# Optimization experiments

Measured on AMD Instinct MI355X. Metric: run time of the kernel, lower is better.

## Reference

```python
import jax, jax.numpy as jnp
import numpy as np

B = 4096          # batch size (scaled up from source's 16)
INPUT_AXIS = 784
LATENT_DIM = 2


def _pdist(x):
    # pairwise euclidean distances in itertools.combinations order (row-major upper triangle)
    sq = jnp.sum(x * x, axis=1)                      # [B]
    d2 = sq[:, None] + sq[None, :] - 2.0 * (x @ x.T)  # [B,B]
    i, j = jnp.triu_indices(x.shape[0], k=1)
    return jnp.sqrt(jnp.maximum(d2[i, j], 0.0))       # [B*(B-1)/2]


def setup_inputs() -> dict:
    key = jax.random.key(0)
    ks = jax.random.split(key, 17)
    dims = [(400, 784), (200, 400), (50, 200), (2, 50),
            (50, 2), (200, 50), (400, 200), (784, 400)]
    names = ['fc1', 'fc1_1', 'fc1_2', 'fc2', 'fc3', 'fc3_1', 'fc3_2', 'fc4']
    inp = {'x': jax.random.uniform(ks[0], (B, 1, 28, 28), dtype=jnp.float32)}
    for idx, (nm, (o, i)) in enumerate(zip(names, dims)):
        bound = 1.0 / np.sqrt(i)
        inp[nm + '_w'] = jax.random.uniform(ks[1 + 2 * idx], (o, i), jnp.float32, -bound, bound)
        inp[nm + '_b'] = jax.random.uniform(ks[2 + 2 * idx], (o,), jnp.float32, -bound, bound)
    return inp


def reference(x, fc1_w, fc1_b, fc1_1_w, fc1_1_b, fc1_2_w, fc1_2_b, fc2_w, fc2_b,
              fc3_w, fc3_b, fc3_1_w, fc3_1_b, fc3_2_w, fc3_2_b, fc4_w, fc4_b):
    lin = lambda h, w, b: h @ w.T + b
    lrelu = jax.nn.leaky_relu  # default slope 0.01, matches F.leaky_relu
    x2 = x.reshape(-1, INPUT_AXIS)                       # [B,784]
    h = lrelu(lin(x2, fc1_w, fc1_b))
    h = lrelu(lin(h, fc1_1_w, fc1_1_b))
    h = lrelu(lin(h, fc1_2_w, fc1_2_b))                  # encoder out [B,50]
    z = lin(jnp.tanh(h), fc2_w, fc2_b)                   # [B,2]
    y = lrelu(lin(z, fc3_w, fc3_b))
    y = lrelu(lin(y, fc3_1_w, fc3_1_b))
    y = lrelu(lin(y, fc3_2_w, fc3_2_b))
    y = jax.nn.sigmoid(lin(y, fc4_w, fc4_b))             # [B,784]
    y_img = y.reshape(B, 1, 28, 28)
    in_diff = _pdist(x2)
    lat_diff = _pdist(z)
    out_diff = _pdist(y.reshape(B, INPUT_AXIS))
    return (y_img, in_diff, lat_diff, out_diff, z)
```

## Files before the change

### kernel.cpp

```cpp
#include <hip/hip_runtime.h>
#include <math.h>

#define NB 4096
#define DIMX 784

typedef __attribute__((ext_vector_type(8))) short bf16x8;
typedef __attribute__((ext_vector_type(4))) float f32x4;

__device__ __forceinline__ float lrelu_f(float v) { return v >= 0.f ? v : 0.01f * v; }

__device__ __forceinline__ void split1(float x, short& hi_s, short& lo_s) {
    unsigned u = __float_as_uint(x);
    unsigned hib = (u + 0x7FFFu + ((u >> 16) & 1u)) & 0xFFFF0000u;
    float hif = __uint_as_float(hib);
    float lo = x - hif;
    unsigned ul = __float_as_uint(lo);
    unsigned lob = (ul + 0x7FFFu + ((ul >> 16) & 1u)) >> 16;
    hi_s = (short)(hib >> 16);
    lo_s = (short)lob;
}

#define GLL(srcp, dstp) __builtin_amdgcn_global_load_lds( \
    (const __attribute__((address_space(1))) void*)(srcp), \
    (__attribute__((address_space(3))) void*)(dstp), 16, 0, 0)


__global__ __launch_bounds__(256) void prep_all(
    const float* __restrict__ w1, const float* __restrict__ w11,
    const float* __restrict__ w32, const float* __restrict__ w4,
    short* __restrict__ o1, short* __restrict__ o11,
    short* __restrict__ o32, short* __restrict__ o4,
    const float* __restrict__ X, short* __restrict__ Xs,
    float* __restrict__ sqx, float* __restrict__ sqy)
{
    const int bid = blockIdx.x;
    const int t = threadIdx.x;
    if (bid < 3920) {
        const float* W; short* O; int N, K, NP, KP, base;
        if (bid < 1600)      { W = w1;  O = o1;  N = 400; K = 784; NP = 512; KP = 800; base = 0; }
        else if (bid < 2016) { W = w11; O = o11; N = 200; K = 400; NP = 256; KP = 416; base = 1600; }
        else if (bid < 2464) { W = w32; O = o32; N = 400; K = 200; NP = 512; KP = 224; base = 2016; }
        else                 { W = w4;  O = o4;  N = 784; K = 400; NP = 896; KP = 416; base = 2464; }
        const int idx = (bid - base) * 256 + t;
        if (idx >= NP * KP) return;
        const int r = idx / KP, k = idx - r * KP;
        short hi = 0, lo = 0;
        if (r < N && k < K) split1(W[(size_t)r * K + k], hi, lo);
        O[(size_t)r * 2 * KP + k]      = hi;
        O[(size_t)r * 2 * KP + KP + k] = lo;
    } else {
        const int r = bid - 3920;
        float s = 0.f;
        if (t < 200) {
            const int k0 = t * 4;
            short h[4] = {0, 0, 0, 0}, l[4] = {0, 0, 0, 0};
            if (k0 < 784) {
                float4 v = *(const float4*)(X + (size_t)r * 784 + k0);
                split1(v.x, h[0], l[0]); split1(v.y, h[1], l[1]);
                split1(v.z, h[2], l[2]); split1(v.w, h[3], l[3]);
                s = v.x * v.x + v.y * v.y + v.z * v.z + v.w * v.w;
            }
            *(uint2*)&Xs[(size_t)r * 1600 + k0]       = *(const uint2*)h;
            *(uint2*)&Xs[(size_t)r * 1600 + 800 + k0] = *(const uint2*)l;
        }
        __shared__ float red[256];
        red[t] = s;
        __syncthreads();
        for (int off = 128; off > 0; off >>= 1) {
            if (t < off) red[t] += red[t + off];
            __syncthreads();
        }
        if (t == 0) { sqx[r] = red[0]; sqy[r] = 0.f; }
    }
}

template<int ACT, bool WF32, bool WSPLIT, bool WROWSQ>
__global__ __launch_bounds__(256) void gemm3_64(
    const short* __restrict__ As_g, const short* __restrict__ Ws_g,
    const float* __restrict__ bias, float* __restrict__ C,
    short* __restrict__ Cs, int N, int KPi, int nchunk, int KPo,
    float* __restrict__ sqy)
{
    __shared__ short L[2][12288];
    const int tid = threadIdx.x;
    const int w = tid >> 6, lane = tid & 63;
    const int wc = w;
    const int m0 = blockIdx.y * 64, n0 = blockIdx.x * 128;
    const int frow = lane & 15;
    const int fk_sw = (((lane >> 4) ^ ((lane >> 1) & 3))) * 8;
    const int srow = tid >> 2;
    const int scol_sw = (((tid & 3) ^ ((tid >> 3) & 3))) * 8;
    const int RS = 2 * KPi;
    const int ld0 = w * 512;

    const short* gA  = As_g + (size_t)(m0 + srow) * RS + scol_sw;
    const short* gB0 = Ws_g + (size_t)(n0 + srow) * RS + scol_sw;
    const short* gB1 = gB0 + (size_t)64 * RS;

    f32x4 acc[4][2] = {};

    auto stage = [&](int buf, int km) {
        GLL(gA  + km,       &L[buf][ld0]);
        GLL(gA  + KPi + km, &L[buf][2048 + ld0]);
        GLL(gB0 + km,       &L[buf][4096 + ld0]);
        GLL(gB1 + km,       &L[buf][6144 + ld0]);
        GLL(gB0 + KPi + km, &L[buf][8192 + ld0]);
        GLL(gB1 + KPi + km, &L[buf][10240 + ld0]);
    };

    stage(0, 0);
    asm volatile("s_waitcnt vmcnt(0)" ::: "memory");
    __builtin_amdgcn_s_barrier();
    int buf = 0;
    #pragma unroll 1
    for (int cc = 0; cc < nchunk; ++cc) {
        if (cc + 1 < nchunk) {
            stage(buf ^ 1, (cc + 1) * 32);
            asm volatile("s_waitcnt vmcnt(6)" ::: "memory");
        } else {
            asm volatile("s_waitcnt vmcnt(0)" ::: "memory");
        }
        __builtin_amdgcn_s_barrier();

        bf16x8 ah[4], al[4], bh[2], bl[2];
        #pragma unroll
        for (int m = 0; m < 4; ++m) {
            const int ro = (m * 16 + frow) * 32 + fk_sw;
            ah[m] = *(const bf16x8*)&L[buf][ro];
            al[m] = *(const bf16x8*)&L[buf][2048 + ro];
        }
        #pragma unroll
        for (int n = 0; n < 2; ++n) {
            const int ro = (wc * 32 + n * 16 + frow) * 32 + fk_sw;
            bh[n] = *(const bf16x8*)&L[buf][4096 + ro];
            bl[n] = *(const bf16x8*)&L[buf][8192 + ro];
        }
        #pragma unroll
        for (int m = 0; m < 4; ++m)
            #pragma unroll
            for (int n = 0; n < 2; ++n) {
                acc[m][n] = __builtin_amdgcn_mfma_f32_16x16x32_bf16(ah[m], bh[n], acc[m][n], 0, 0, 0);
                acc[m][n] = __builtin_amdgcn_mfma_f32_16x16x32_bf16(ah[m], bl[n], acc[m][n], 0, 0, 0);
                acc[m][n] = __builtin_amdgcn_mfma_f32_16x16x32_bf16(al[m], bh[n], acc[m][n], 0, 0, 0);
            }
        __builtin_amdgcn_s_barrier();
        buf ^= 1;
    }

    const int col0 = lane & 15;
    const int row4 = (lane >> 4) * 4;

    float* rowsum = (float*)&L[0][0];
    if (WROWSQ) {
        __syncthreads();
        if (tid < 64) rowsum[tid] = 0.f;
        __syncthreads();
    }

    #pragma unroll
    for (int m = 0; m < 4; ++m) {
        #pragma unroll
        for (int r = 0; r < 4; ++r) {
            const int gm = m0 + m * 16 + row4 + r;
            float vsq = 0.f;
            #pragma unroll
            for (int n = 0; n < 2; ++n) {
                const int gn = n0 + wc * 32 + n * 16 + col0;
                float v = 0.f;
                if (gn < N) {
                    v = acc[m][n][r] + bias[gn];
                    if (ACT == 1)      v = lrelu_f(v);
                    else if (ACT == 2) v = 1.f / (1.f + expf(-v));
                }
                if (WF32 && gn < N) C[(size_t)gm * N + gn] = v;
                if (WSPLIT && gn < KPo) {
                    short hi, lo; split1(v, hi, lo);
                    Cs[(size_t)gm * 2 * KPo + gn]       = hi;
                    Cs[(size_t)gm * 2 * KPo + KPo + gn] = lo;
                }
                if (WROWSQ) vsq = fmaf(v, v, vsq);
            }
            if (WROWSQ) atomicAdd(&rowsum[m * 16 + row4 + r], vsq);
        }
    }
    if (WROWSQ) {
        __syncthreads();
        if (tid < 64) atomicAdd(&sqy[m0 + tid], rowsum[tid]);
    }
}

__global__ __launch_bounds__(256) void fused_mid(
    const float* __restrict__ h2, const float* __restrict__ W12,
    const float* __restrict__ b12, const float* __restrict__ W2,
    const float* __restrict__ b2,  const float* __restrict__ W3,
    const float* __restrict__ b3,  const float* __restrict__ W31,
    const float* __restrict__ b31, float* __restrict__ z_out,
    short* __restrict__ y2s)
{
    __shared__ float wbuf[200 * 51];
    __shared__ float hl[16 * 201];
    __shared__ float h3l[16 * 51];
    __shared__ float y1l[16 * 51];
    __shared__ float zl[16 * 2];
    __shared__ float w2l[100], w3l[100];
    __shared__ float b12l[50], b2l[2], b3l[50], b31l[200];
    const int t = threadIdx.x;
    const int r0 = blockIdx.x * 16;

    for (int i = t; i < 50 * 200; i += 256) { int n = i / 200, k = i - n * 200; wbuf[n * 201 + k] = W12[i]; }
    for (int i = t; i < 16 * 200; i += 256) { int r = i / 200, k = i - r * 200; hl[r * 201 + k] = h2[(size_t)(r0 + r) * 200 + k]; }
    for (int i = t; i < 100; i += 256) { w2l[i] = W2[i]; w3l[i] = W3[i]; }
    if (t < 50)  { b12l[t] = b12[t]; b3l[t] = b3[t]; }
    if (t < 2)   b2l[t] = b2[t];
    if (t < 200) b31l[t] = b31[t];
    __syncthreads();

    for (int i = t; i < 16 * 50; i += 256) {
        int r = i / 50, n = i - r * 50;
        float s = b12l[n];
        #pragma unroll 4
        for (int k = 0; k < 200; ++k) s = fmaf(hl[r * 201 + k], wbuf[n * 201 + k], s);
        h3l[r * 51 + n] = tanhf(lrelu_f(s));
    }
    __syncthreads();

    if (t < 32) {
        int r = t >> 1, n = t & 1;
        float s = b2l[n];
        #pragma unroll
        for (int k = 0; k < 50; ++k) s = fmaf(h3l[r * 51 + k], w2l[n * 50 + k], s);
        zl[r * 2 + n] = s;
        z_out[(size_t)(r0 + r) * 2 + n] = s;
    }
    for (int i = t; i < 200 * 50; i += 256) { int n = i / 50, k = i - n * 50; wbuf[n * 51 + k] = W31[i]; }
    __syncthreads();

    for (int i = t; i < 16 * 50; i += 256) {
        int r = i / 50, n = i - r * 50;
        float s = fmaf(zl[r * 2], w3l[n * 2], fmaf(zl[r * 2 + 1], w3l[n * 2 + 1], b3l[n]));
        y1l[r * 51 + n] = lrelu_f(s);
    }
    __syncthreads();

    for (int i = t; i < 16 * 224; i += 256) {
        int r = i / 224, n = i - r * 224;
        float v = 0.f;
        if (n < 200) {
            float s = b31l[n];
            #pragma unroll
            for (int k = 0; k < 50; ++k) s = fmaf(y1l[r * 51 + k], wbuf[n * 51 + k], s);
            v = lrelu_f(s);
        }
        short hi, lo; split1(v, hi, lo);
        const size_t gm = r0 + r;
        y2s[gm * 448 + n]       = hi;
        y2s[gm * 448 + 224 + n] = lo;
    }
}

__global__ __launch_bounds__(256, 4) void pdist_all(
    const short* __restrict__ xs, const short* __restrict__ ys,
    const float* __restrict__ sqx, const float* __restrict__ sqy,
    const float* __restrict__ Z, float* __restrict__ in_diff,
    float* __restrict__ out_diff, float* __restrict__ lat_diff)
{
    __shared__ short L[4][4096];
    const int tid = threadIdx.x;
    const int orig = blockIdx.x;

    if (orig < 528) {
        const int b = (orig & 7) * 66 + (orig >> 3);
        int rem = b, ti = 0;
        while (rem >= 32 - ti) { rem -= 32 - ti; ++ti; }
        const int tj = ti + rem;

        const int w = tid >> 6, lane = tid & 63;
        const int wr = w >> 1, wc = w & 1;
        const int frow = lane & 15;
        const int fk_sw = (((lane >> 4) ^ ((lane >> 1) & 3))) * 8;
        const int srow = tid >> 2;
        const int scol_sw = (((tid & 3) ^ ((tid >> 3) & 3))) * 8;
        const int i0 = ti * 128, j0 = tj * 128;
        const int ld0 = w * 512;

        const short* gA = ys + (size_t)(i0 + srow) * 1600 + scol_sw;
        const short* gB = ys + (size_t)(j0 + srow) * 1600 + scol_sw;
        const size_t half = (size_t)64 * 1600;

        f32x4 acc[4][4] = {};

        #pragma unroll 1
        for (int cc = 0; cc < 25; ++cc) {
            const int km = cc * 32;
            __syncthreads();
            GLL(gA + km,       &L[0][ld0]);   GLL(gA + half + km,       &L[0][2048 + ld0]);
            GLL(gB + km,       &L[2][ld0]);   GLL(gB + half + km,       &L[2][2048 + ld0]);
            GLL(gA + 800 + km, &L[1][ld0]);   GLL(gA + half + 800 + km, &L[1][2048 + ld0]);
            GLL(gB + 800 + km, &L[3][ld0]);   GLL(gB + half + 800 + km, &L[3][2048 + ld0]);
            __syncthreads();

            bf16x8 ah[4], bh[4];
            #pragma unroll
            for (int m = 0; m < 4; ++m)
                ah[m] = *(const bf16x8*)&L[0][(wr * 64 + m * 16 + frow) * 32 + fk_sw];
            #pragma unroll
            for (int n = 0; n < 4; ++n)
                bh[n] = *(const bf16x8*)&L[2][(wc * 64 + n * 16 + frow) * 32 + fk_sw];
            #pragma unroll
            for (int m = 0; m < 4; ++m)
                #pragma unroll
                for (int n = 0; n < 4; ++n)
                    acc[m][n] = __builtin_amdgcn_mfma_f32_16x16x32_bf16(ah[m], bh[n], acc[m][n], 0, 0, 0);

            bf16x8 al[4], bl[4];
            #pragma unroll
            for (int n = 0; n < 4; ++n)
                bl[n] = *(const bf16x8*)&L[3][(wc * 64 + n * 16 + frow) * 32 + fk_sw];
            #pragma unroll
            for (int m = 0; m < 4; ++m)
                #pragma unroll
                for (int n = 0; n < 4; ++n)
                    acc[m][n] = __builtin_amdgcn_mfma_f32_16x16x32_bf16(ah[m], bl[n], acc[m][n], 0, 0, 0);
            #pragma unroll
            for (int m = 0; m < 4; ++m)
                al[m] = *(const bf16x8*)&L[1][(wr * 64 + m * 16 + frow) * 32 + fk_sw];
            #pragma unroll
            for (int m = 0; m < 4; ++m)
                #pragma unroll
                for (int n = 0; n < 4; ++n)
                    acc[m][n] = __builtin_amdgcn_mfma_f32_16x16x32_bf16(al[m], bh[n], acc[m][n], 0, 0, 0);
        }

        const int col0 = lane & 15;
        const int row4 = (lane >> 4) * 4;
        float sqj_v[4];
        #pragma unroll
        for (int n = 0; n < 4; ++n)
            sqj_v[n] = sqy[j0 + wc * 64 + n * 16 + col0];

        #pragma unroll
        for (int m = 0; m < 4; ++m) {
            #pragma unroll
            for (int r = 0; r < 4; ++r) {
                const int gi = i0 + wr * 64 + m * 16 + row4 + r;
                const float sqi = sqy[gi];
                const int rowbase = (gi * (2 * NB - 1 - gi)) / 2 - gi - 1;
                #pragma unroll
                for (int n = 0; n < 4; ++n) {
                    const int gj = j0 + wc * 64 + n * 16 + col0;
                    if (gj > gi) {
                        float d2 = sqi + sqj_v[n] - 2.f * acc[m][n][r];
                        out_diff[rowbase + gj] = sqrtf(fmaxf(d2, 0.f));
                    }
                }
            }
        }
    } else if (orig < 1056) {
        const int o = orig - 528;
        const int b = (o & 7) * 66 + (o >> 3);
        int rem = b, ti = 0;
        while (rem >= 32 - ti) { rem -= 32 - ti; ++ti; }
        const int tj = ti + rem;

        const int w = tid >> 6, lane = tid & 63;
        const int wr = w >> 1, wc = w & 1;
        const int frow = lane & 15;
        const int fk_sw = (((lane >> 4) ^ ((lane >> 1) & 3))) * 8;
        const int srow = tid >> 2;
        const int scol_sw = (((tid & 3) ^ ((tid >> 3) & 3))) * 8;
        const int i0 = ti * 128, j0 = tj * 128;
        const int ld0 = w * 512;

        const short* gA = xs + (size_t)(i0 + srow) * 1600 + scol_sw;
        const short* gB = xs + (size_t)(j0 + srow) * 1600 + scol_sw;
        const size_t half = (size_t)64 * 1600;

        f32x4 acc[4][4] = {};

        auto stage = [&](int buf, int km) {
            short* dA = buf ? &L[2][0] : &L[0][0];
            short* dB = buf ? &L[3][0] : &L[1][0];
            GLL(gA + km,        dA + ld0);   GLL(gA + half + km, dA + 2048 + ld0);
            GLL(gB + km,        dB + ld0);   GLL(gB + half + km, dB + 2048 + ld0);
        };

        stage(0, 0);
        asm volatile("s_waitcnt vmcnt(0)" ::: "memory");
        __builtin_amdgcn_s_barrier();
        int buf = 0;
        #pragma unroll 1
        for (int cc = 0; cc < 25; ++cc) {
            if (cc < 24) {
                stage(buf ^ 1, (cc + 1) * 32);
                asm volatile("s_waitcnt vmcnt(4)" ::: "memory");
            } else {
                asm volatile("s_waitcnt vmcnt(0)" ::: "memory");
            }
            __builtin_amdgcn_s_barrier();

            const short* SA = buf ? &L[2][0] : &L[0][0];
            const short* SB = buf ? &L[3][0] : &L[1][0];
            bf16x8 a[4], bb[4];
            #pragma unroll
            for (int m = 0; m < 4; ++m)
                a[m] = *(const bf16x8*)&SA[(wr * 64 + m * 16 + frow) * 32 + fk_sw];
            #pragma unroll
            for (int n = 0; n < 4; ++n)
                bb[n] = *(const bf16x8*)&SB[(wc * 64 + n * 16 + frow) * 32 + fk_sw];
            #pragma unroll
            for (int m = 0; m < 4; ++m)
                #pragma unroll
                for (int n = 0; n < 4; ++n)
                    acc[m][n] = __builtin_amdgcn_mfma_f32_16x16x32_bf16(a[m], bb[n], acc[m][n], 0, 0, 0);
            __builtin_amdgcn_s_barrier();
            buf ^= 1;
        }

        const int col0 = lane & 15;
        const int row4 = (lane >> 4) * 4;
        float sqj_v[4];
        #pragma unroll
        for (int n = 0; n < 4; ++n)
            sqj_v[n] = sqx[j0 + wc * 64 + n * 16 + col0];
        #pragma unroll
        for (int m = 0; m < 4; ++m) {
            #pragma unroll
            for (int r = 0; r < 4; ++r) {
                const int gi = i0 + wr * 64 + m * 16 + row4 + r;
                const float sqi = sqx[gi];
                const int rowbase = (gi * (2 * NB - 1 - gi)) / 2 - gi - 1;
                #pragma unroll
                for (int n = 0; n < 4; ++n) {
                    const int gj = j0 + wc * 64 + n * 16 + col0;
                    if (gj > gi) {
                        float d2 = sqi + sqj_v[n] - 2.f * acc[m][n][r];
                        in_diff[rowbase + gj] = sqrtf(fmaxf(d2, 0.f));
                    }
                }
            }
        }
    } else {
        const int o = orig - 1056;
        const int b = (o & 7) * 66 + (o >> 3);
        int rem = b, ti = 0;
        while (rem >= 32 - ti) { rem -= 32 - ti; ++ti; }
        const int tj = ti + rem;
        const int i0 = ti * 128, j0 = tj * 128;

        float* zi = (float*)&L[0][0];
        float* zj = (float*)&L[0][512];
        if (tid < 128) {
            *(float2*)&zi[tid * 2] = *(const float2*)&Z[(size_t)(i0 + tid) * 2];
        } else {
            const int r = tid - 128;
            *(float2*)&zj[r * 2] = *(const float2*)&Z[(size_t)(j0 + r) * 2];
        }
        __syncthreads();

        const int ty = tid >> 4;
        const int tx = tid & 15;
        #pragma unroll
        for (int ii = 0; ii < 8; ++ii) {
            const int li = ty * 8 + ii;
            const int gi = i0 + li;
            const int rowbase = (gi * (2 * NB - 1 - gi)) / 2 - gi - 1;
            const float zi0 = zi[li * 2], zi1 = zi[li * 2 + 1];
            #pragma unroll
            for (int jj = 0; jj < 8; ++jj) {
                const int lj = tx * 8 + jj;
                const int gj = j0 + lj;
                if (gj > gi) {
                    float d0 = zi0 - zj[lj * 2];
                    float d1 = zi1 - zj[lj * 2 + 1];
                    lat_diff[rowbase + gj] = sqrtf(fmaf(d0, d0, d1 * d1));
                }
            }
        }
    }
}

extern "C" void kernel_launch(void* const* d_in, const int* in_sizes, int n_in,
                              void* d_out, int out_size, void* d_ws, size_t ws_size,
                              hipStream_t stream)
{
    const float* x       = (const float*)d_in[0];
    const float* fc1_w   = (const float*)d_in[1];
    const float* fc1_b   = (const float*)d_in[2];
    const float* fc11_w  = (const float*)d_in[3];
    const float* fc11_b  = (const float*)d_in[4];
    const float* fc12_w  = (const float*)d_in[5];
    const float* fc12_b  = (const float*)d_in[6];
    const float* fc2_w   = (const float*)d_in[7];
    const float* fc2_b   = (const float*)d_in[8];
    const float* fc3_w   = (const float*)d_in[9];
    const float* fc3_b   = (const float*)d_in[10];
    const float* fc31_w  = (const float*)d_in[11];
    const float* fc31_b  = (const float*)d_in[12];
    const float* fc32_w  = (const float*)d_in[13];
    const float* fc32_b  = (const float*)d_in[14];
    const float* fc4_w   = (const float*)d_in[15];
    const float* fc4_b   = (const float*)d_in[16];

    float* out = (float*)d_out;
    float* y        = out;
    float* in_diff  = out + 3211264;
    float* lat_diff = out + 11597824;
    float* out_diff = out + 19984384;
    float* z        = out + 28370944;

    float* ws   = (float*)d_ws;
    float* h2   = ws;
    float* h3u  = h2  + (size_t)4096 * 200;
    float* y1u  = h3u + (size_t)4096 * 50;
    float* sqx  = y1u + (size_t)4096 * 50;
    float* sqy  = sqx + 4096;
    short* xs   = (short*)(sqy + 4096);
    short* ys   = xs  + (size_t)NB * 1600;
    short* w1s  = ys  + (size_t)NB * 1600;
    short* w11s = w1s  + (size_t)512 * 1600;
    short* w32s = w11s + (size_t)256 * 832;
    short* w4s  = w32s + (size_t)512 * 448;
    short* h1s  = w4s  + (size_t)896 * 832;
    short* y3s  = h1s;
    short* y2s  = h1s  + (size_t)4096 * 832;

    const dim3 blk(256);

    prep_all<<<dim3(8016), blk, 0, stream>>>(
        fc1_w, fc11_w, fc32_w, fc4_w, w1s, w11s, w32s, w4s, x, xs, sqx, sqy);
    gemm3_64<1, false, true, false><<<dim3(4, 64), blk, 0, stream>>>(
        xs, w1s, fc1_b, nullptr, h1s, 400, 800, 25, 416, nullptr);
    gemm3_64<1, true, false, false><<<dim3(2, 64), blk, 0, stream>>>(
        h1s, w11s, fc11_b, h2, nullptr, 200, 416, 13, 0, nullptr);
    fused_mid<<<dim3(256), blk, 0, stream>>>(
        h2, fc12_w, fc12_b, fc2_w, fc2_b, fc3_w, fc3_b, fc31_w, fc31_b, z, y2s);
    gemm3_64<1, false, true, false><<<dim3(4, 64), blk, 0, stream>>>(
        y2s, w32s, fc32_b, nullptr, y3s, 400, 224, 7, 416, nullptr);
    gemm3_64<2, true, true, true><<<dim3(7, 64), blk, 0, stream>>>(
        y3s, w4s, fc4_b, y, ys, 784, 416, 13, 800, sqy);
    pdist_all<<<dim3(1584), blk, 0, stream>>>(
        xs, ys, sqx, sqy, z, in_diff, out_diff, lat_diff);
}
```

Before: 225.9 us.

## Co-schedule input pdist tiles with the fc1 GEMM in one launch

Computing in_diff depends only on x, so its 528 tile blocks now run in the same launch as the fc1 GEMM (new fc1_mix kernel, 784 blocks). The final pdist kernel keeps only the output and latent distance work. The aim is to fill the GPU during the small fc1 GEMM (256 blocks) and shorten the long tail of the last kernel. fc1 uses a dedicated 64x128 split-bf16 tile with three MFMAs per step. The mixed kernel's larger LDS footprint (48KB) may lower occupancy for the pdist blocks.

```diff
diff --git a/kernel.cpp b/kernel.cpp
--- a/kernel.cpp
+++ b/kernel.cpp
@@ -189,6 +189,181 @@
     }
 }
 
+__global__ __launch_bounds__(256) void fc1_mix(
+    const short* __restrict__ xs, const short* __restrict__ w1s,
+    const float* __restrict__ fc1_b, short* __restrict__ h1s,
+    const float* __restrict__ sqx, float* __restrict__ in_diff)
+{
+    __shared__ short L[24576];
+    const int tid = threadIdx.x;
+    const int w = tid >> 6, lane = tid & 63;
+    const int frow = lane & 15;
+    const int fk_sw = (((lane >> 4) ^ ((lane >> 1) & 3))) * 8;
+    const int srow = tid >> 2;
+    const int scol_sw = (((tid & 3) ^ ((tid >> 3) & 3))) * 8;
+    const int ld0 = w * 512;
+    const int col0 = lane & 15;
+    const int row4 = (lane >> 4) * 4;
+    const int bid = blockIdx.x;
+
+    if (bid < 256) {
+        const int wc = w;
+        const int m0 = (bid >> 2) * 64, n0 = (bid & 3) * 128;
+        const int RS = 1600;
+
+        const short* gA  = xs  + (size_t)(m0 + srow) * RS + scol_sw;
+        const short* gB0 = w1s + (size_t)(n0 + srow) * RS + scol_sw;
+        const short* gB1 = gB0 + (size_t)64 * RS;
+
+        f32x4 acc[4][2] = {};
+
+        auto stage = [&](int buf, int km) {
+            short* B = L + buf * 12288;
+            GLL(gA  + km,       B + ld0);
+            GLL(gA  + 800 + km, B + 2048 + ld0);
+            GLL(gB0 + km,       B + 4096 + ld0);
+            GLL(gB1 + km,       B + 6144 + ld0);
+            GLL(gB0 + 800 + km, B + 8192 + ld0);
+            GLL(gB1 + 800 + km, B + 10240 + ld0);
+        };
+
+        stage(0, 0);
+        asm volatile("s_waitcnt vmcnt(0)" ::: "memory");
+        __builtin_amdgcn_s_barrier();
+        int buf = 0;
+        #pragma unroll 1
+        for (int cc = 0; cc < 25; ++cc) {
+            if (cc < 24) {
+                stage(buf ^ 1, (cc + 1) * 32);
+                asm volatile("s_waitcnt vmcnt(6)" ::: "memory");
+            } else {
+                asm volatile("s_waitcnt vmcnt(0)" ::: "memory");
+            }
+            __builtin_amdgcn_s_barrier();
+
+            const short* B = L + buf * 12288;
+            bf16x8 ah[4], al[4], bh[2], bl[2];
+            #pragma unroll
+            for (int m = 0; m < 4; ++m) {
+                const int ro = (m * 16 + frow) * 32 + fk_sw;
+                ah[m] = *(const bf16x8*)&B[ro];
+                al[m] = *(const bf16x8*)&B[2048 + ro];
+            }
+            #pragma unroll
+            for (int n = 0; n < 2; ++n) {
+                const int ro = (wc * 32 + n * 16 + frow) * 32 + fk_sw;
+                bh[n] = *(const bf16x8*)&B[4096 + ro];
+                bl[n] = *(const bf16x8*)&B[8192 + ro];
+            }
+            #pragma unroll
+            for (int m = 0; m < 4; ++m)
+                #pragma unroll
+                for (int n = 0; n < 2; ++n) {
+                    acc[m][n] = __builtin_amdgcn_mfma_f32_16x16x32_bf16(ah[m], bh[n], acc[m][n], 0, 0, 0);
+                    acc[m][n] = __builtin_amdgcn_mfma_f32_16x16x32_bf16(ah[m], bl[n], acc[m][n], 0, 0, 0);
+                    acc[m][n] = __builtin_amdgcn_mfma_f32_16x16x32_bf16(al[m], bh[n], acc[m][n], 0, 0, 0);
+                }
+            __builtin_amdgcn_s_barrier();
+            buf ^= 1;
+        }
+
+        #pragma unroll
+        for (int m = 0; m < 4; ++m) {
+            #pragma unroll
+            for (int r = 0; r < 4; ++r) {
+                const int gm = m0 + m * 16 + row4 + r;
+                #pragma unroll
+                for (int n = 0; n < 2; ++n) {
+                    const int gn = n0 + wc * 32 + n * 16 + col0;
+                    float v = 0.f;
+                    if (gn < 400) v = lrelu_f(acc[m][n][r] + fc1_b[gn]);
+                    if (gn < 416) {
+                        short hi, lo; split1(v, hi, lo);
+                        h1s[(size_t)gm * 832 + gn]       = hi;
+                        h1s[(size_t)gm * 832 + 416 + gn] = lo;
+                    }
+                }
+            }
+        }
+    } else {
+        const int o = bid - 256;
+        const int b = (o & 7) * 66 + (o >> 3);
+        int rem = b, ti = 0;
+        while (rem >= 32 - ti) { rem -= 32 - ti; ++ti; }
+        const int tj = ti + rem;
+
+        const int wr = w >> 1, wc = w & 1;
+        const int i0 = ti * 128, j0 = tj * 128;
+
+        const short* gA = xs + (size_t)(i0 + srow) * 1600 + scol_sw;
+        const short* gB = xs + (size_t)(j0 + srow) * 1600 + scol_sw;
+        const size_t half = (size_t)64 * 1600;
+
+        f32x4 acc[4][4] = {};
+
+        auto stage = [&](int buf, int km) {
+            short* dA = buf ? L + 8192  : L + 0;
+            short* dB = buf ? L + 12288 : L + 4096;
+            GLL(gA + km,        dA + ld0);   GLL(gA + half + km, dA + 2048 + ld0);
+            GLL(gB + km,        dB + ld0);   GLL(gB + half + km, dB + 2048 + ld0);
+        };
+
+        stage(0, 0);
+        asm volatile("s_waitcnt vmcnt(0)" ::: "memory");
+        __builtin_amdgcn_s_barrier();
+        int buf = 0;
+        #pragma unroll 1
+        for (int cc = 0; cc < 25; ++cc) {
+            if (cc < 24) {
+                stage(buf ^ 1, (cc + 1) * 32);
+                asm volatile("s_waitcnt vmcnt(4)" ::: "memory");
+            } else {
+                asm volatile("s_waitcnt vmcnt(0)" ::: "memory");
+            }
+            __builtin_amdgcn_s_barrier();
+
+            const short* SA = buf ? L + 8192  : L + 0;
+            const short* SB = buf ? L + 12288 : L + 4096;
+            bf16x8 a[4], bb[4];
+            #pragma unroll
+            for (int m = 0; m < 4; ++m)
+                a[m] = *(const bf16x8*)&SA[(wr * 64 + m * 16 + frow) * 32 + fk_sw];
+            #pragma unroll
+            for (int n = 0; n < 4; ++n)
+                bb[n] = *(const bf16x8*)&SB[(wc * 64 + n * 16 + frow) * 32 + fk_sw];
+            #pragma unroll
+            for (int m = 0; m < 4; ++m)
+                #pragma unroll
+                for (int n = 0; n < 4; ++n)
+                    acc[m][n] = __builtin_amdgcn_mfma_f32_16x16x32_bf16(a[m], bb[n], acc[m][n], 0, 0, 0);
+            __builtin_amdgcn_s_barrier();
+            buf ^= 1;
+        }
+
+        float sqj_v[4];
+        #pragma unroll
+        for (int n = 0; n < 4; ++n)
+            sqj_v[n] = sqx[j0 + wc * 64 + n * 16 + col0];
+        #pragma unroll
+        for (int m = 0; m < 4; ++m) {
+            #pragma unroll
+            for (int r = 0; r < 4; ++r) {
+                const int gi = i0 + wr * 64 + m * 16 + row4 + r;
+                const float sqi = sqx[gi];
+                const int rowbase = (gi * (2 * NB - 1 - gi)) / 2 - gi - 1;
+                #pragma unroll
+                for (int n = 0; n < 4; ++n) {
+                    const int gj = j0 + wc * 64 + n * 16 + col0;
+                    if (gj > gi) {
+                        float d2 = sqi + sqj_v[n] - 2.f * acc[m][n][r];
+                        in_diff[rowbase + gj] = sqrtf(fmaxf(d2, 0.f));
+                    }
+                }
+            }
+        }
+    }
+}
+
 __global__ __launch_bounds__(256) void fused_mid(
     const float* __restrict__ h2, const float* __restrict__ W12,
     const float* __restrict__ b12, const float* __restrict__ W2,
@@ -258,11 +433,10 @@
     }
 }
 
-__global__ __launch_bounds__(256, 4) void pdist_all(
-    const short* __restrict__ xs, const short* __restrict__ ys,
-    const float* __restrict__ sqx, const float* __restrict__ sqy,
-    const float* __restrict__ Z, float* __restrict__ in_diff,
-    float* __restrict__ out_diff, float* __restrict__ lat_diff)
+__global__ __launch_bounds__(256, 4) void pdist_hz(
+    const short* __restrict__ ys, const float* __restrict__ sqy,
+    const float* __restrict__ Z, float* __restrict__ out_diff,
+    float* __restrict__ lat_diff)
 {
     __shared__ short L[4][4096];
     const int tid = threadIdx.x;
@@ -355,92 +529,8 @@
                 }
             }
         }
-    } else if (orig < 1056) {
+    } else {
         const int o = orig - 528;
-        const int b = (o & 7) * 66 + (o >> 3);
-        int rem = b, ti = 0;
-        while (rem >= 32 - ti) { rem -= 32 - ti; ++ti; }
-        const int tj = ti + rem;
-
-        const int w = tid >> 6, lane = tid & 63;
-        const int wr = w >> 1, wc = w & 1;
-        const int frow = lane & 15;
-        const int fk_sw = (((lane >> 4) ^ ((lane >> 1) & 3))) * 8;
-        const int srow = tid >> 2;
-        const int scol_sw = (((tid & 3) ^ ((tid >> 3) & 3))) * 8;
-        const int i0 = ti * 128, j0 = tj * 128;
-        const int ld0 = w * 512;
-
-        const short* gA = xs + (size_t)(i0 + srow) * 1600 + scol_sw;
-        const short* gB = xs + (size_t)(j0 + srow) * 1600 + scol_sw;
-        const size_t half = (size_t)64 * 1600;
-
-        f32x4 acc[4][4] = {};
-
-        auto stage = [&](int buf, int km) {
-            short* dA = buf ? &L[2][0] : &L[0][0];
-            short* dB = buf ? &L[3][0] : &L[1][0];
-            GLL(gA + km,        dA + ld0);   GLL(gA + half + km, dA + 2048 + ld0);
-            GLL(gB + km,        dB + ld0);   GLL(gB + half + km, dB + 2048 + ld0);
-        };
-
-        stage(0, 0);
-        asm volatile("s_waitcnt vmcnt(0)" ::: "memory");
-        __builtin_amdgcn_s_barrier();
-        int buf = 0;
-        #pragma unroll 1
-        for (int cc = 0; cc < 25; ++cc) {
-            if (cc < 24) {
-                stage(buf ^ 1, (cc + 1) * 32);
-                asm volatile("s_waitcnt vmcnt(4)" ::: "memory");
-            } else {
-                asm volatile("s_waitcnt vmcnt(0)" ::: "memory");
-            }
-            __builtin_amdgcn_s_barrier();
-
-            const short* SA = buf ? &L[2][0] : &L[0][0];
-            const short* SB = buf ? &L[3][0] : &L[1][0];
-            bf16x8 a[4], bb[4];
-            #pragma unroll
-            for (int m = 0; m < 4; ++m)
-                a[m] = *(const bf16x8*)&SA[(wr * 64 + m * 16 + frow) * 32 + fk_sw];
-            #pragma unroll
-            for (int n = 0; n < 4; ++n)
-                bb[n] = *(const bf16x8*)&SB[(wc * 64 + n * 16 + frow) * 32 + fk_sw];
-            #pragma unroll
-            for (int m = 0; m < 4; ++m)
-                #pragma unroll
-                for (int n = 0; n < 4; ++n)
-                    acc[m][n] = __builtin_amdgcn_mfma_f32_16x16x32_bf16(a[m], bb[n], acc[m][n], 0, 0, 0);
-            __builtin_amdgcn_s_barrier();
-            buf ^= 1;
-        }
-
-        const int col0 = lane & 15;
-        const int row4 = (lane >> 4) * 4;
-        float sqj_v[4];
-        #pragma unroll
-        for (int n = 0; n < 4; ++n)
-            sqj_v[n] = sqx[j0 + wc * 64 + n * 16 + col0];
-        #pragma unroll
-        for (int m = 0; m < 4; ++m) {
-            #pragma unroll
-            for (int r = 0; r < 4; ++r) {
-                const int gi = i0 + wr * 64 + m * 16 + row4 + r;
-                const float sqi = sqx[gi];
-                const int rowbase = (gi * (2 * NB - 1 - gi)) / 2 - gi - 1;
-                #pragma unroll
-                for (int n = 0; n < 4; ++n) {
-                    const int gj = j0 + wc * 64 + n * 16 + col0;
-                    if (gj > gi) {
-                        float d2 = sqi + sqj_v[n] - 2.f * acc[m][n][r];
-                        in_diff[rowbase + gj] = sqrtf(fmaxf(d2, 0.f));
-                    }
-                }
-            }
-        }
-    } else {
-        const int o = orig - 1056;
         const int b = (o & 7) * 66 + (o >> 3);
         int rem = b, ti = 0;
         while (rem >= 32 - ti) { rem -= 32 - ti; ++ti; }
@@ -528,8 +618,7 @@
 
     prep_all<<<dim3(8016), blk, 0, stream>>>(
         fc1_w, fc11_w, fc32_w, fc4_w, w1s, w11s, w32s, w4s, x, xs, sqx, sqy);
-    gemm3_64<1, false, true, false><<<dim3(4, 64), blk, 0, stream>>>(
-        xs, w1s, fc1_b, nullptr, h1s, 400, 800, 25, 416, nullptr);
+    fc1_mix<<<dim3(784), blk, 0, stream>>>(xs, w1s, fc1_b, h1s, sqx, in_diff);
     gemm3_64<1, true, false, false><<<dim3(2, 64), blk, 0, stream>>>(
         h1s, w11s, fc11_b, h2, nullptr, 200, 416, 13, 0, nullptr);
     fused_mid<<<dim3(256), blk, 0, stream>>>(
@@ -538,6 +627,5 @@
         y2s, w32s, fc32_b, nullptr, y3s, 400, 224, 7, 416, nullptr);
     gemm3_64<2, true, true, true><<<dim3(7, 64), blk, 0, stream>>>(
         y3s, w4s, fc4_b, y, ys, 784, 416, 13, 800, sqy);
-    pdist_all<<<dim3(1584), blk, 0, stream>>>(
-        xs, ys, sqx, sqy, z, in_diff, out_diff, lat_diff);
+    pdist_hz<<<dim3(1056), blk, 0, stream>>>(ys, sqy, z, out_diff, lat_diff);
 }
```

Measured after the change: 235.8 us. 4.4% more time.
